# Kernel optimization log

Measured on AMD Instinct MI355X. Metric: run time of the kernel, lower is better.

## Reference

```python
import jax, jax.numpy as jnp
import numpy as np
from jax import lax

BN_EPS = 1e-3  # keras BatchNormalization default epsilon
DN = ('NHWC', 'HWIO', 'NHWC')


def ste_sign(x):
    # larq ste_sign forward: sign with sign(0) -> +1
    return jnp.where(x >= 0, 1.0, -1.0).astype(x.dtype)


def bn_inference(x, beta, mean, var):
    # scale=False -> no gamma, center=True -> beta
    return (x - mean) * lax.rsqrt(var + BN_EPS) + beta


def setup_inputs() -> dict:
    key = jax.random.key(0)
    ks = jax.random.split(key, 8)
    C = 256
    x = jax.random.normal(ks[0], (32, 56, 56, C), dtype=jnp.float32)
    w1 = jax.random.normal(ks[1], (3, 3, C, C), dtype=jnp.float32) * 0.05
    w2 = jax.random.normal(ks[2], (3, 3, C, C), dtype=jnp.float32) * 0.05
    beta1 = jax.random.normal(ks[3], (C,), dtype=jnp.float32) * 0.1
    beta2 = jax.random.normal(ks[4], (C,), dtype=jnp.float32) * 0.1
    mean1 = jax.random.normal(ks[5], (C,), dtype=jnp.float32) * 0.1
    mean2 = jax.random.normal(ks[6], (C,), dtype=jnp.float32) * 0.1
    var1 = jax.random.uniform(ks[7], (C,), dtype=jnp.float32, minval=0.5, maxval=1.5)
    var2 = jax.random.uniform(jax.random.fold_in(key, 7), (C,), dtype=jnp.float32, minval=0.5, maxval=1.5)
    return {"x": x, "w1": w1, "beta1": beta1, "mean1": mean1, "var1": var1,
            "w2": w2, "beta2": beta2, "mean2": mean2, "var2": var2}


def reference(x, w1, beta1, mean1, var1, w2, beta2, mean2, var2):
    # conv_1: quantized input and quantized weights (XNOR conv), stride 1, SAME
    h = lax.conv_general_dilated(ste_sign(x), ste_sign(w1), (1, 1), 'SAME',
                                 dimension_numbers=DN)
    h = bn_inference(h, beta1, mean1, var1)
    # conv_2: quantized input and weights
    h = lax.conv_general_dilated(ste_sign(h), ste_sign(w2), (1, 1), 'SAME',
                                 dimension_numbers=DN)
    # max pool 2x2 stride 2
    h = lax.reduce_window(h, -jnp.inf, lax.max, (1, 2, 2, 1), (1, 2, 2, 1), 'VALID')
    h = bn_inference(h, beta2, mean2, var2)
    return h
```

## Files before the change

### kernel.cpp

```cpp
#include <hip/hip_runtime.h>
#include <stdint.h>

#define BN_EPS 1e-3f

constexpr int Bn = 32, H = 56, Wd = 56, C = 256;
constexpr int NSLOT = 232;
typedef int v4i __attribute__((ext_vector_type(4)));

__device__ __forceinline__ int imax(int a, int b) { return a > b ? a : b; }

__global__ __launch_bounds__(256) void k_sign_x(const float* __restrict__ x,
                                                int8_t* __restrict__ xs, int n4) {
  int i = blockIdx.x * 256 + threadIdx.x;
  if (i >= n4) return;
  float4 v = ((const float4*)x)[i];
  char4 s;
  s.x = v.x >= 0.f ? 1 : -1;
  s.y = v.y >= 0.f ? 1 : -1;
  s.z = v.z >= 0.f ? 1 : -1;
  s.w = v.w >= 0.f ? 1 : -1;
  ((char4*)xs)[i] = s;
}

__global__ __launch_bounds__(256) void k_sign_wT2(const float* __restrict__ w,
                                                  uint32_t* __restrict__ wt) {
  int u = blockIdx.x * 256 + threadIdx.x;
  int f = u >> 8, r = u & 255;
  int l = r >> 2, w4 = r & 3;
  int grp = l >> 4, lid = l & 15;
  int tap = f >> 6, icq = (f >> 4) & 3, ocg = f & 15;
  int oc = ocg * 16 + lid;
  uint32_t pk = 0;
#pragma unroll
  for (int j = 0; j < 4; ++j) {
    int ic = icq * 64 + grp * 16 + w4 * 4 + j;
    float v = w[((size_t)(tap * 256 + ic)) * 256 + oc];
    pk |= (v >= 0.f ? 0x01u : 0xFFu) << (8 * j);
  }
  wt[u] = pk;
}

template <int MODE, int MS, int MSB>
__device__ __forceinline__ void conv_body(
    const int8_t* As, const int8_t* __restrict__ wT2, int wn, int lane,
    const float* __restrict__ beta, const float* __restrict__ mean,
    const float* __restrict__ var, int8_t* __restrict__ hs,
    float* __restrict__ outp, int b, int rp)
{
  const int grp = lane >> 4, lid = lane & 15;
  const int wbase = wn * 128;
  const int cstg = grp << 4;

  int sb[MS], sb7[MS];
#pragma unroll
  for (int ms = 0; ms < MS; ++ms) {
    const int m = (MSB + ms) * 16 + lid;
    sb[ms] = (m & 1) * 58 + (m >> 1);
    sb7[ms] = sb[ms] & 7;
  }

  const int8_t* bpl = wT2 + (size_t)wn * 8192 + (size_t)lane * 16;

  v4i acc[MS][8];
#pragma unroll
  for (int i = 0; i < MS; ++i)
#pragma unroll
    for (int j = 0; j < 8; ++j) acc[i][j] = (v4i){0, 0, 0, 0};

#pragma unroll 1
  for (int ky = 0; ky < 3; ++ky) {
#pragma unroll 1
    for (int kx = 0; kx < 3; ++kx) {
      const int D = ky * 58 + kx;
      const int8_t* bt = bpl + (size_t)(ky * 3 + kx) * 65536;
      int slin[MS], key[MS];
#pragma unroll
      for (int ms = 0; ms < MS; ++ms) {
        slin[ms] = (sb[ms] + D) << 8;
        key[ms] = ((sb7[ms] + D) & 7) << 4;
      }
#pragma unroll
      for (int icq = 0; icq < 4; ++icq) {
        v4i bf[8];
#pragma unroll
        for (int ns = 0; ns < 8; ++ns)
          bf[ns] = *(const v4i*)(bt + icq * 16384 + ns * 1024);
        v4i af[MS];
#pragma unroll
        for (int ms = 0; ms < MS; ++ms)
          af[ms] = *(const v4i*)(As + slin[ms] + ((cstg + icq * 64) ^ key[ms]));
        __builtin_amdgcn_s_setprio(1);
#pragma unroll
        for (int ms = 0; ms < MS; ++ms)
#pragma unroll
          for (int ns = 0; ns < 8; ++ns)
            acc[ms][ns] = __builtin_amdgcn_mfma_i32_16x16x64_i8(
                af[ms], bf[ns], acc[ms][ns], 0, 0, 0);
        __builtin_amdgcn_s_setprio(0);
      }
    }
  }

  const int rA = rp * 2;
  if (MODE == 0) {
#pragma unroll
    for (int ns = 0; ns < 8; ++ns) {
      const int oc = wbase + ns * 16 + lid;
      const float mu = mean[oc], rs = rsqrtf(var[oc] + BN_EPS), be = beta[oc];
#pragma unroll
      for (int ms = 0; ms < MS; ++ms)
#pragma unroll
        for (int q = 0; q < 4; ++q) {
          const int m = (MSB + ms) * 16 + grp * 4 + q;
          const int lr = m & 1, col = m >> 1;
          const float bnv = ((float)acc[ms][ns][q] - mu) * rs + be;
          hs[(((size_t)(b * 56 + rA + lr)) * 56 + col) * 256 + oc] =
              bnv >= 0.f ? (int8_t)1 : (int8_t)-1;
        }
    }
  } else {
#pragma unroll
    for (int ns = 0; ns < 8; ++ns) {
      const int oc = wbase + ns * 16 + lid;
      const float mu = mean[oc], rs = rsqrtf(var[oc] + BN_EPS), be = beta[oc];
#pragma unroll
      for (int ms = 0; ms < MS; ++ms) {
        const int mx = imax(imax(acc[ms][ns][0], acc[ms][ns][1]),
                            imax(acc[ms][ns][2], acc[ms][ns][3]));
        const int j = (MSB + ms) * 4 + grp;
        outp[(((size_t)(b * 28 + rp)) * 28 + j) * 256 + oc] =
            ((float)mx - mu) * rs + be;
      }
    }
  }
}

template <int MODE>
__global__ __launch_bounds__(256, 2) void k_conv(
    const int8_t* __restrict__ src, const int8_t* __restrict__ wT2,
    const float* __restrict__ beta, const float* __restrict__ mean,
    const float* __restrict__ var,
    int8_t* __restrict__ hs, float* __restrict__ outp)
{
  const int t = threadIdx.x;
  const int rp = blockIdx.x;
  const int b = blockIdx.y;
  const int rr0 = rp * 2;

  __shared__ __align__(16) int8_t As[NSLOT * 256];

  for (int i = t; i < NSLOT * 16; i += 256) {
    const int s = i >> 4, c = i & 15;
    const int lr = s / 58, colst = s - lr * 58;
    const int sr = rr0 + lr - 1, sc = colst - 1;
    uint4 v;
    v.x = v.y = v.z = v.w = 0u;
    if ((unsigned)sr < 56u && (unsigned)sc < 56u)
      v = *(const uint4*)(src + (((size_t)(b * 56 + sr)) * 56 + sc) * 256 + c * 16);
    *(uint4*)(As + (s << 8) + ((c << 4) ^ ((s & 7) << 4))) = v;
  }
  __syncthreads();

  const int lane = t & 63;
  const int wv = t >> 6;
  const int wm = wv >> 1, wn = wv & 1;
  if (wm == 0)
    conv_body<MODE, 4, 0>(As, wT2, wn, lane, beta, mean, var, hs, outp, b, rp);
  else
    conv_body<MODE, 3, 4>(As, wT2, wn, lane, beta, mean, var, hs, outp, b, rp);
}

extern "C" void kernel_launch(void* const* d_in, const int* in_sizes, int n_in,
                              void* d_out, int out_size, void* d_ws, size_t ws_size,
                              hipStream_t stream) {
  const float* x     = (const float*)d_in[0];
  const float* w1    = (const float*)d_in[1];
  const float* beta1 = (const float*)d_in[2];
  const float* mean1 = (const float*)d_in[3];
  const float* var1  = (const float*)d_in[4];
  const float* w2    = (const float*)d_in[5];
  const float* beta2 = (const float*)d_in[6];
  const float* mean2 = (const float*)d_in[7];
  const float* var2  = (const float*)d_in[8];
  float* out = (float*)d_out;

  const size_t NPIX = (size_t)Bn * H * Wd * C;
  int8_t* xs  = (int8_t*)d_ws;
  int8_t* hs  = xs + NPIX;
  int8_t* w1t = hs + NPIX;
  int8_t* w2t = w1t + 589824;

  k_sign_x<<<dim3((int)(NPIX / 4 / 256)), 256, 0, stream>>>(x, xs, (int)(NPIX / 4));
  k_sign_wT2<<<dim3(576), 256, 0, stream>>>(w1, (uint32_t*)w1t);
  k_sign_wT2<<<dim3(576), 256, 0, stream>>>(w2, (uint32_t*)w2t);
  k_conv<0><<<dim3(28, Bn), 256, 0, stream>>>(xs, w1t, beta1, mean1, var1, hs, nullptr);
  k_conv<1><<<dim3(28, Bn), 256, 0, stream>>>(hs, w2t, beta2, mean2, var2, nullptr, out);
}
```

Measured before the change: 150.5 us.

## Switch conv to 32x32x32 int8 MFMA with double-buffered operand loads

Replaces the 16x16x64 int8 MFMA tiling with 32x32x32 MFMA tiles (2x4 per wave) and repacks the sign weights into a matching layout. The K loop is flattened into 72 steps over tap and 32-channel slices, with A and B fragments ping-ponged so the loads for the next step are issued before the current MFMAs. This aims to cut LDS and global fragment traffic per MFMA and to hide load latency. In exchange the 32-row M tiles cover 128 pixels where only 112 are valid, so some MFMA work is spent on padding that has to be masked in the epilogue. The LDS buffer is enlarged to cover those padded reads.

```diff
diff --git a/kernel.cpp b/kernel.cpp
--- a/kernel.cpp
+++ b/kernel.cpp
@@ -4,8 +4,9 @@
 #define BN_EPS 1e-3f
 
 constexpr int Bn = 32, H = 56, Wd = 56, C = 256;
-constexpr int NSLOT = 232;
+constexpr int NSLOT = 240;
 typedef int v4i __attribute__((ext_vector_type(4)));
+typedef int v16i __attribute__((ext_vector_type(16)));
 
 __device__ __forceinline__ int imax(int a, int b) { return a > b ? a : b; }
 
@@ -22,122 +23,28 @@
   ((char4*)xs)[i] = s;
 }
 
-__global__ __launch_bounds__(256) void k_sign_wT2(const float* __restrict__ w,
+__global__ __launch_bounds__(256) void k_sign_wT3(const float* __restrict__ w,
                                                   uint32_t* __restrict__ wt) {
   int u = blockIdx.x * 256 + threadIdx.x;
-  int f = u >> 8, r = u & 255;
-  int l = r >> 2, w4 = r & 3;
-  int grp = l >> 4, lid = l & 15;
-  int tap = f >> 6, icq = (f >> 4) & 3, ocg = f & 15;
-  int oc = ocg * 16 + lid;
+  int w4 = u & 3;
+  int l = (u >> 2) & 63;
+  int nsub = (u >> 8) & 7;
+  int ics = (u >> 11) & 7;
+  int tap = u >> 14;
+  int oc = nsub * 32 + (l & 31);
   uint32_t pk = 0;
 #pragma unroll
   for (int j = 0; j < 4; ++j) {
-    int ic = icq * 64 + grp * 16 + w4 * 4 + j;
+    int ic = ics * 32 + (l >> 5) * 16 + w4 * 4 + j;
     float v = w[((size_t)(tap * 256 + ic)) * 256 + oc];
     pk |= (v >= 0.f ? 0x01u : 0xFFu) << (8 * j);
   }
   wt[u] = pk;
 }
 
-template <int MODE, int MS, int MSB>
-__device__ __forceinline__ void conv_body(
-    const int8_t* As, const int8_t* __restrict__ wT2, int wn, int lane,
-    const float* __restrict__ beta, const float* __restrict__ mean,
-    const float* __restrict__ var, int8_t* __restrict__ hs,
-    float* __restrict__ outp, int b, int rp)
-{
-  const int grp = lane >> 4, lid = lane & 15;
-  const int wbase = wn * 128;
-  const int cstg = grp << 4;
-
-  int sb[MS], sb7[MS];
-#pragma unroll
-  for (int ms = 0; ms < MS; ++ms) {
-    const int m = (MSB + ms) * 16 + lid;
-    sb[ms] = (m & 1) * 58 + (m >> 1);
-    sb7[ms] = sb[ms] & 7;
-  }
-
-  const int8_t* bpl = wT2 + (size_t)wn * 8192 + (size_t)lane * 16;
-
-  v4i acc[MS][8];
-#pragma unroll
-  for (int i = 0; i < MS; ++i)
-#pragma unroll
-    for (int j = 0; j < 8; ++j) acc[i][j] = (v4i){0, 0, 0, 0};
-
-#pragma unroll 1
-  for (int ky = 0; ky < 3; ++ky) {
-#pragma unroll 1
-    for (int kx = 0; kx < 3; ++kx) {
-      const int D = ky * 58 + kx;
-      const int8_t* bt = bpl + (size_t)(ky * 3 + kx) * 65536;
-      int slin[MS], key[MS];
-#pragma unroll
-      for (int ms = 0; ms < MS; ++ms) {
-        slin[ms] = (sb[ms] + D) << 8;
-        key[ms] = ((sb7[ms] + D) & 7) << 4;
-      }
-#pragma unroll
-      for (int icq = 0; icq < 4; ++icq) {
-        v4i bf[8];
-#pragma unroll
-        for (int ns = 0; ns < 8; ++ns)
-          bf[ns] = *(const v4i*)(bt + icq * 16384 + ns * 1024);
-        v4i af[MS];
-#pragma unroll
-        for (int ms = 0; ms < MS; ++ms)
-          af[ms] = *(const v4i*)(As + slin[ms] + ((cstg + icq * 64) ^ key[ms]));
-        __builtin_amdgcn_s_setprio(1);
-#pragma unroll
-        for (int ms = 0; ms < MS; ++ms)
-#pragma unroll
-          for (int ns = 0; ns < 8; ++ns)
-            acc[ms][ns] = __builtin_amdgcn_mfma_i32_16x16x64_i8(
-                af[ms], bf[ns], acc[ms][ns], 0, 0, 0);
-        __builtin_amdgcn_s_setprio(0);
-      }
-    }
-  }
-
-  const int rA = rp * 2;
-  if (MODE == 0) {
-#pragma unroll
-    for (int ns = 0; ns < 8; ++ns) {
-      const int oc = wbase + ns * 16 + lid;
-      const float mu = mean[oc], rs = rsqrtf(var[oc] + BN_EPS), be = beta[oc];
-#pragma unroll
-      for (int ms = 0; ms < MS; ++ms)
-#pragma unroll
-        for (int q = 0; q < 4; ++q) {
-          const int m = (MSB + ms) * 16 + grp * 4 + q;
-          const int lr = m & 1, col = m >> 1;
-          const float bnv = ((float)acc[ms][ns][q] - mu) * rs + be;
-          hs[(((size_t)(b * 56 + rA + lr)) * 56 + col) * 256 + oc] =
-              bnv >= 0.f ? (int8_t)1 : (int8_t)-1;
-        }
-    }
-  } else {
-#pragma unroll
-    for (int ns = 0; ns < 8; ++ns) {
-      const int oc = wbase + ns * 16 + lid;
-      const float mu = mean[oc], rs = rsqrtf(var[oc] + BN_EPS), be = beta[oc];
-#pragma unroll
-      for (int ms = 0; ms < MS; ++ms) {
-        const int mx = imax(imax(acc[ms][ns][0], acc[ms][ns][1]),
-                            imax(acc[ms][ns][2], acc[ms][ns][3]));
-        const int j = (MSB + ms) * 4 + grp;
-        outp[(((size_t)(b * 28 + rp)) * 28 + j) * 256 + oc] =
-            ((float)mx - mu) * rs + be;
-      }
-    }
-  }
-}
-
 template <int MODE>
 __global__ __launch_bounds__(256, 2) void k_conv(
-    const int8_t* __restrict__ src, const int8_t* __restrict__ wT2,
+    const int8_t* __restrict__ src, const int8_t* __restrict__ wT3,
     const float* __restrict__ beta, const float* __restrict__ mean,
     const float* __restrict__ var,
     int8_t* __restrict__ hs, float* __restrict__ outp)
@@ -149,7 +56,7 @@
 
   __shared__ __align__(16) int8_t As[NSLOT * 256];
 
-  for (int i = t; i < NSLOT * 16; i += 256) {
+  for (int i = t; i < 232 * 16; i += 256) {
     const int s = i >> 4, c = i & 15;
     const int lr = s / 58, colst = s - lr * 58;
     const int sr = rr0 + lr - 1, sc = colst - 1;
@@ -164,10 +71,115 @@
   const int lane = t & 63;
   const int wv = t >> 6;
   const int wm = wv >> 1, wn = wv & 1;
-  if (wm == 0)
-    conv_body<MODE, 4, 0>(As, wT2, wn, lane, beta, mean, var, hs, outp, b, rp);
-  else
-    conv_body<MODE, 3, 4>(As, wT2, wn, lane, beta, mean, var, hs, outp, b, rp);
+  const int col31 = lane & 31, kh = lane >> 5;
+  const int kbyte = kh * 16;
+
+  const int m0 = (wm * 2 + 0) * 32 + col31;
+  const int m1 = (wm * 2 + 1) * 32 + col31;
+  const int sb0 = (m0 & 1) * 58 + (m0 >> 1);
+  const int sb1 = (m1 & 1) * 58 + (m1 >> 1);
+
+  const int8_t* bpl = wT3 + (size_t)wn * 4096 + (size_t)lane * 16;
+
+  v16i acc[2][4];
+#pragma unroll
+  for (int i = 0; i < 2; ++i)
+#pragma unroll
+    for (int j = 0; j < 4; ++j) acc[i][j] = (v16i)0;
+
+#define LOADB(dst, st)                                                     \
+  {                                                                        \
+    const int8_t* p_ = bpl + (size_t)(st) * 8192;                          \
+    dst[0] = *(const v4i*)(p_);                                            \
+    dst[1] = *(const v4i*)(p_ + 1024);                                     \
+    dst[2] = *(const v4i*)(p_ + 2048);                                     \
+    dst[3] = *(const v4i*)(p_ + 3072);                                     \
+  }
+
+#define LOADA(dst, st)                                                     \
+  {                                                                        \
+    const int tap_ = (st) >> 3, ics_ = (st) & 7;                           \
+    const int ky_ = tap_ / 3, kx_ = tap_ - 3 * ky_;                        \
+    const int D_ = ky_ * 58 + kx_;                                         \
+    const int ko_ = ics_ * 32 + kbyte;                                     \
+    const int s0_ = sb0 + D_, s1_ = sb1 + D_;                              \
+    dst[0] = *(const v4i*)(As + (s0_ << 8) + (ko_ ^ ((s0_ & 7) << 4)));    \
+    dst[1] = *(const v4i*)(As + (s1_ << 8) + (ko_ ^ ((s1_ & 7) << 4)));    \
+  }
+
+#define MFMA8(af, bf)                                                      \
+  __builtin_amdgcn_s_setprio(1);                                           \
+  _Pragma("unroll") for (int ms = 0; ms < 2; ++ms)                         \
+  _Pragma("unroll") for (int ns = 0; ns < 4; ++ns)                         \
+      acc[ms][ns] = __builtin_amdgcn_mfma_i32_32x32x32_i8(                 \
+          af[ms], bf[ns], acc[ms][ns], 0, 0, 0);                           \
+  __builtin_amdgcn_s_setprio(0);
+
+  v4i afA[2], afB[2], bfA[4], bfB[4];
+  LOADA(afA, 0)
+  LOADB(bfA, 0)
+
+#pragma unroll 1
+  for (int i = 0; i < 36; ++i) {
+    const int s = 2 * i;
+    const int s1 = s + 1;
+    const int s2 = (s + 2 > 71) ? 71 : s + 2;
+    LOADA(afB, s1)
+    LOADB(bfB, s1)
+    MFMA8(afA, bfA)
+    LOADA(afA, s2)
+    LOADB(bfA, s2)
+    MFMA8(afB, bfB)
+  }
+
+#undef MFMA8
+#undef LOADA
+#undef LOADB
+
+  const int rA = rp * 2;
+  const int wbase = wn * 128;
+  if (MODE == 0) {
+#pragma unroll
+    for (int ns = 0; ns < 4; ++ns) {
+      const int oc = wbase + ns * 32 + col31;
+      const float mu = mean[oc], rs = rsqrtf(var[oc] + BN_EPS), be = beta[oc];
+#pragma unroll
+      for (int msl = 0; msl < 2; ++msl) {
+        const int msub = wm * 2 + msl;
+#pragma unroll
+        for (int reg = 0; reg < 16; ++reg) {
+          const int m = msub * 32 + (reg & 3) + 8 * (reg >> 2) + 4 * kh;
+          const int col = m >> 1, row = m & 1;
+          if (col < 56) {
+            const float bnv = ((float)acc[msl][ns][reg] - mu) * rs + be;
+            hs[(((size_t)(b * 56 + rA + row)) * 56 + col) * 256 + oc] =
+                bnv >= 0.f ? (int8_t)1 : (int8_t)-1;
+          }
+        }
+      }
+    }
+  } else {
+#pragma unroll
+    for (int ns = 0; ns < 4; ++ns) {
+      const int oc = wbase + ns * 32 + col31;
+      const float mu = mean[oc], rs = rsqrtf(var[oc] + BN_EPS), be = beta[oc];
+#pragma unroll
+      for (int msl = 0; msl < 2; ++msl) {
+        const int msub = wm * 2 + msl;
+#pragma unroll
+        for (int g = 0; g < 4; ++g) {
+          const int jj = msub * 8 + 2 * g + kh;
+          if (jj < 28) {
+            const int mx =
+                imax(imax(acc[msl][ns][4 * g + 0], acc[msl][ns][4 * g + 1]),
+                     imax(acc[msl][ns][4 * g + 2], acc[msl][ns][4 * g + 3]));
+            outp[(((size_t)(b * 28 + rp)) * 28 + jj) * 256 + oc] =
+                ((float)mx - mu) * rs + be;
+          }
+        }
+      }
+    }
+  }
 }
 
 extern "C" void kernel_launch(void* const* d_in, const int* in_sizes, int n_in,
@@ -191,8 +203,8 @@
   int8_t* w2t = w1t + 589824;
 
   k_sign_x<<<dim3((int)(NPIX / 4 / 256)), 256, 0, stream>>>(x, xs, (int)(NPIX / 4));
-  k_sign_wT2<<<dim3(576), 256, 0, stream>>>(w1, (uint32_t*)w1t);
-  k_sign_wT2<<<dim3(576), 256, 0, stream>>>(w2, (uint32_t*)w2t);
+  k_sign_wT3<<<dim3(576), 256, 0, stream>>>(w1, (uint32_t*)w1t);
+  k_sign_wT3<<<dim3(576), 256, 0, stream>>>(w2, (uint32_t*)w2t);
   k_conv<0><<<dim3(28, Bn), 256, 0, stream>>>(xs, w1t, beta1, mean1, var1, hs, nullptr);
   k_conv<1><<<dim3(28, Bn), 256, 0, stream>>>(hs, w2t, beta2, mean2, var2, nullptr, out);
 }
```

Result: slower. 187.5 us (+24.6%).
